# Kernel optimization log

Measured on AMD Instinct MI355X. Metric: run time of the kernel, lower is better.

The kernel has to match this reference:

```python
import jax, jax.numpy as jnp
import numpy as np

N_WIN = 7
DIM = 128
QK = 128
HEADS = 8
TOPK = 4


def _win(x, n_win):
    # (N, H, W, C) -> (N, n_win*n_win, h, w, C)
    N, H, W, C = x.shape
    h, w = H // n_win, W // n_win
    return x.reshape(N, n_win, h, n_win, w, C).transpose(0, 1, 3, 2, 4, 5).reshape(N, n_win * n_win, h, w, C)


def _unwin(x, n_win):
    # (N, p2, h, w, C) -> (N, H, W, C)
    N, p2, h, w, C = x.shape
    return x.reshape(N, n_win, n_win, h, w, C).transpose(0, 1, 3, 2, 4, 5).reshape(N, n_win * h, n_win * w, C)


def _dwconv(img_nhwc, k, b):
    # depthwise 3x3, SAME padding (LePE)
    x = img_nhwc.transpose(0, 3, 1, 2)
    y = jax.lax.conv_general_dilated(x, k, (1, 1), 'SAME',
                                     dimension_numbers=('NCHW', 'OIHW', 'NCHW'),
                                     feature_group_count=k.shape[0])
    y = y + b[None, :, None, None]
    return y.transpose(0, 2, 3, 1)


def _branch(xw, W, b):
    # xw: (N, p2, h, w, C); QKV linear + pixel/window-level views
    qkv = xw @ W + b
    q, kv = qkv[..., :QK], qkv[..., QK:]
    N, p2, h, w, _ = q.shape
    q_pix = q.reshape(N, p2, h * w, QK)
    kv_pix = kv.reshape(N, p2, h * w, QK + DIM)  # identity kv_down
    q_win = q.mean((2, 3))
    k_win = kv[..., :QK].mean((2, 3))
    return q_pix, kv_pix, q_win, k_win, kv


def _route(q_win, k_win, scale):
    # non-differentiable routing (detach) with Identity emb
    q = jax.lax.stop_gradient(q_win)
    k = jax.lax.stop_gradient(k_win)
    logit = (q * scale) @ k.transpose(0, 2, 1)  # (N, p2, p2)
    top_val, top_idx = jax.lax.top_k(logit, TOPK)
    r_weight = jax.nn.softmax(top_val, axis=-1)  # unused (mul_weight='none')
    return r_weight, top_idx


def _gather(kv_pix, idx):
    # kv_pix: (N, p2, w2, c), idx: (N, p2, K) -> (N, p2, K, w2, c)
    N = kv_pix.shape[0]
    bidx = jnp.arange(N)[:, None, None]
    return kv_pix[bidx, idx]


def _heads_q(q):
    # (N, p2, w2, m*c) -> (N, p2, m, w2, c)
    N, p2, w2, _ = q.shape
    return q.reshape(N, p2, w2, HEADS, -1).transpose(0, 1, 3, 2, 4)


def _heads_kv(kv):
    # (N, p2, K, w2, m*c) -> (N, p2, m, K*w2, c)
    N, p2, K, w2, _ = kv.shape
    return kv.reshape(N, p2, K, w2, HEADS, -1).transpose(0, 1, 4, 2, 3, 5).reshape(N, p2, HEADS, K * w2, -1)


def setup_inputs() -> dict:
    key = jax.random.key(0)
    ks = jax.random.split(key, 6)
    N, H, W = 8, 56, 56
    return {
        'x': jax.random.normal(ks[0], (N, H, W, DIM), jnp.float32),
        'y': jax.random.normal(ks[1], (N, H, W, DIM), jnp.float32),
        'w_qkv_x': jax.random.normal(ks[2], (DIM, 2 * QK + DIM), jnp.float32) * 0.02,
        'b_qkv_x': jnp.zeros((2 * QK + DIM,), jnp.float32),
        'w_qkv_y': jax.random.normal(ks[3], (DIM, 2 * QK + DIM), jnp.float32) * 0.02,
        'b_qkv_y': jnp.zeros((2 * QK + DIM,), jnp.float32),
        'w_lepe_x': jax.random.normal(ks[4], (DIM, 1, 3, 3), jnp.float32) * 0.1,
        'b_lepe_x': jnp.zeros((DIM,), jnp.float32),
        'w_lepe_y': jax.random.normal(ks[5], (DIM, 1, 3, 3), jnp.float32) * 0.1,
        'b_lepe_y': jnp.zeros((DIM,), jnp.float32),
    }


def reference(x, y, w_qkv_x, b_qkv_x, w_qkv_y, b_qkv_y, w_lepe_x, b_lepe_x, w_lepe_y, b_lepe_y):
    scale = QK ** (-0.5)
    N, H, W, C = x.shape
    h, w = H // N_WIN, W // N_WIN
    xw = _win(x, N_WIN)
    yw = _win(y, N_WIN)

    qx_pix, kvx_pix, qx_win, kx_win, kvx = _branch(xw, w_qkv_x, b_qkv_x)
    qy_pix, kvy_pix, qy_win, ky_win, kvy = _branch(yw, w_qkv_y, b_qkv_y)

    lepe_x = _dwconv(_unwin(kvx[..., QK:], N_WIN), w_lepe_x, b_lepe_x)
    lepe_y = _dwconv(_unwin(kvy[..., QK:], N_WIN), w_lepe_y, b_lepe_y)

    _, rx_idx = _route(qx_win, kx_win, scale)
    _, ry_idx = _route(qy_win, ky_win, scale)

    kvx_sel = _gather(kvx_pix, rx_idx)  # (N, p2, K, w2, QK+DIM)
    kvy_sel = _gather(kvy_pix, ry_idx)

    kx_sel, vx_sel = _heads_kv(kvx_sel[..., :QK]), _heads_kv(kvx_sel[..., QK:])
    ky_sel, vy_sel = _heads_kv(kvy_sel[..., :QK]), _heads_kv(kvy_sel[..., QK:])
    qx = _heads_q(qx_pix)
    qy = _heads_q(qy_pix)

    attn_x = jax.nn.softmax(jnp.einsum('bpmqc,bpmkc->bpmqk', qx * scale, kx_sel), axis=-1)
    attn_y = jax.nn.softmax(jnp.einsum('bpmqc,bpmkc->bpmqk', qy * scale, ky_sel), axis=-1)

    # cross attention: x-output uses y's attention weights on x's values, and vice versa
    out_x = jnp.einsum('bpmqk,bpmkc->bpmqc', attn_y, vx_sel)
    out_y = jnp.einsum('bpmqk,bpmkc->bpmqc', attn_x, vy_sel)

    p2 = N_WIN * N_WIN
    out_x = out_x.transpose(0, 1, 3, 2, 4).reshape(N, p2, h, w, DIM)
    out_y = out_y.transpose(0, 1, 3, 2, 4).reshape(N, p2, h, w, DIM)
    out_x = _unwin(out_x, N_WIN) + lepe_x
    out_y = _unwin(out_y, N_WIN) + lepe_y
    return (out_x, out_y)
```

## Files before the change

kernel.cpp:

```cpp
#include <hip/hip_runtime.h>

#define HWD 56
#define NWIN 7
#define P2 49
#define CIN 128
#define COUT 384
#define NB 8
#define SCALE 0.08838834764831843f

typedef __attribute__((ext_vector_type(8))) short bf16x8;
typedef __attribute__((ext_vector_type(4))) float f32x4;
typedef __attribute__((ext_vector_type(8))) unsigned short u16x8;
typedef unsigned short ushort_t;

__device__ inline unsigned short f2bf(float f) {
  unsigned int u = __float_as_uint(f);
  unsigned int r = (u + 0x7fffu + ((u >> 16) & 1u)) >> 16;
  return (unsigned short)r;
}
__device__ inline float bf2f(unsigned short b) {
  return __uint_as_float(((unsigned int)b) << 16);
}

__global__ __launch_bounds__(256) void meanproj_kernel(
    const float* __restrict__ xin, const float* __restrict__ yin,
    const float* __restrict__ Wx, const float* __restrict__ Bx,
    const float* __restrict__ Wy, const float* __restrict__ By,
    ushort_t* __restrict__ xbfx, ushort_t* __restrict__ xbfy,
    float* __restrict__ qwx, float* __restrict__ kwx,
    float* __restrict__ qwy, float* __restrict__ kwy)
{
  const int p = blockIdx.x, n = blockIdx.y, br = blockIdx.z;
  const float* X  = br ? yin : xin;
  const float* W  = br ? Wy  : Wx;
  const float* Bv = br ? By  : Bx;
  ushort_t* xb = (br ? xbfy : xbfx) + (size_t)(n * P2 + p) * 64 * CIN;
  float* qw = br ? qwy : qwx;
  float* kw = br ? kwy : kwx;

  __shared__ float sm[2][128];
  __shared__ float mxs[128];
  const int t = threadIdx.x;
  const int wr = p / NWIN, wc = p % NWIN;
  const int ch = t & 127, half = t >> 7;

  float s = 0.f;
#pragma unroll 4
  for (int i = 0; i < 32; ++i) {
    int pix = half * 32 + i;
    int a = wr * 8 + (pix >> 3), b = wc * 8 + (pix & 7);
    float v = X[(((size_t)n * HWD + a) * HWD + b) * CIN + ch];
    s += v;
    xb[pix * CIN + ch] = f2bf(v);
  }
  sm[half][ch] = s;
  __syncthreads();
  if (t < 128) mxs[t] = (sm[0][t] + sm[1][t]) * (1.f / 64.f);
  __syncthreads();

  float acc = Bv[t];
#pragma unroll 8
  for (int k = 0; k < 128; ++k) acc = fmaf(mxs[k], W[(size_t)k * COUT + t], acc);
  if (t < 128) qw[(n * P2 + p) * 128 + t] = acc;
  else         kw[(n * P2 + p) * 128 + (t - 128)] = acc;
}

__global__ __launch_bounds__(128) void wt_kernel(
    const float* __restrict__ Wx, const float* __restrict__ Wy,
    ushort_t* __restrict__ Wtx, ushort_t* __restrict__ Wty)
{
  const int br = blockIdx.y;
  const float* W = br ? Wy : Wx;
  ushort_t* Wt = br ? Wty : Wtx;
  const int c = blockIdx.x * 128 + threadIdx.x;
  for (int k8 = 0; k8 < 128; k8 += 8) {
    u16x8 buf;
#pragma unroll
    for (int i = 0; i < 8; ++i) buf[i] = f2bf(W[(size_t)(k8 + i) * COUT + c]);
    *(u16x8*)&Wt[(size_t)c * 128 + k8] = buf;
  }
}

__global__ __launch_bounds__(256) void route_kernel(
    const float* __restrict__ qwx, const float* __restrict__ kwx,
    const float* __restrict__ qwy, const float* __restrict__ kwy,
    int* __restrict__ idxx, int* __restrict__ idxy)
{
  const int br = blockIdx.x, n = blockIdx.y;
  const float* qw = br ? qwy : qwx;
  const float* kw = br ? kwy : kwx;
  int* idx = br ? idxy : idxx;

  __shared__ float qs[P2][128];
  __shared__ float ks[P2][128];
  __shared__ float ls[P2][52];
  const int t = threadIdx.x;
  for (int e = t; e < P2 * 128; e += 256) {
    qs[e >> 7][e & 127] = qw[(size_t)n * P2 * 128 + e];
    ks[e >> 7][e & 127] = kw[(size_t)n * P2 * 128 + e];
  }
  __syncthreads();
  for (int pair = t; pair < P2 * P2; pair += 256) {
    int r = pair / P2, j = pair % P2;
    float d = 0.f;
#pragma unroll
    for (int c4 = 0; c4 < 32; ++c4) {
      float4 a = *(const float4*)&qs[r][c4 * 4];
      float4 b = *(const float4*)&ks[j][c4 * 4];
      d = fmaf(a.x, b.x, d); d = fmaf(a.y, b.y, d);
      d = fmaf(a.z, b.z, d); d = fmaf(a.w, b.w, d);
    }
    ls[r][j] = d;
  }
  __syncthreads();
  if (t < P2) {
    int ch[4];
    for (int s = 0; s < 4; ++s) {
      float best = -1e30f; int bi = 0;
      for (int j = 0; j < P2; ++j) {
        bool taken = false;
        for (int u = 0; u < s; ++u) taken = taken || (ch[u] == j);
        if (!taken && ls[t][j] > best) { best = ls[t][j]; bi = j; }
      }
      ch[s] = bi;
      idx[((size_t)n * P2 + t) * 4 + s] = bi;
    }
  }
}

#define AS 136
__global__ __launch_bounds__(256) void qkv_gemm_kernel(
    const ushort_t* __restrict__ xbfx, const ushort_t* __restrict__ xbfy,
    const ushort_t* __restrict__ Wtx, const ushort_t* __restrict__ Wty,
    const float* __restrict__ Bx, const float* __restrict__ By,
    ushort_t* __restrict__ Qpx, ushort_t* __restrict__ Qpy,
    ushort_t* __restrict__ Kpx, ushort_t* __restrict__ Kpy,
    ushort_t* __restrict__ Vcx, ushort_t* __restrict__ Vcy,
    ushort_t* __restrict__ Vpx, ushort_t* __restrict__ Vpy)
{
  const int mt = blockIdx.x, nt = blockIdx.y, br = blockIdx.z;
  const ushort_t* Xb = br ? xbfy : xbfx;
  const ushort_t* Wt = br ? Wty : Wtx;
  const float* Bv = br ? By : Bx;

  __shared__ ushort_t a_s[128 * AS];
  __shared__ ushort_t b_s[128 * AS];

  const int t = threadIdx.x;
#pragma unroll
  for (int it = 0; it < 8; ++it) {
    int row = it * 16 + (t >> 4);
    int e8 = (t & 15) * 8;
    *(u16x8*)&a_s[row * AS + e8] = *(const u16x8*)&Xb[((size_t)mt * 128 + row) * 128 + e8];
    *(u16x8*)&b_s[row * AS + e8] = *(const u16x8*)&Wt[((size_t)nt * 128 + row) * 128 + e8];
  }
  __syncthreads();

  const int wv = t >> 6, wm = wv >> 1, wn = wv & 1;
  const int lane = t & 63, qd = lane >> 4, m16 = lane & 15;

  f32x4 acc[4][4];
#pragma unroll
  for (int i = 0; i < 4; ++i)
#pragma unroll
    for (int j = 0; j < 4; ++j) acc[i][j] = (f32x4){0.f, 0.f, 0.f, 0.f};

#pragma unroll
  for (int ks = 0; ks < 4; ++ks) {
    bf16x8 af[4], bfr[4];
#pragma unroll
    for (int fi = 0; fi < 4; ++fi)
      af[fi] = *(const bf16x8*)&a_s[(wm * 64 + fi * 16 + m16) * AS + ks * 32 + qd * 8];
#pragma unroll
    for (int fj = 0; fj < 4; ++fj)
      bfr[fj] = *(const bf16x8*)&b_s[(wn * 64 + fj * 16 + m16) * AS + ks * 32 + qd * 8];
#pragma unroll
    for (int fi = 0; fi < 4; ++fi)
#pragma unroll
      for (int fj = 0; fj < 4; ++fj)
        acc[fi][fj] = __builtin_amdgcn_mfma_f32_16x16x32_bf16(bfr[fj], af[fi], acc[fi][fj], 0, 0, 0);
  }

  const int gw = mt * 2 + wm;
  const float scl = (nt == 0) ? SCALE : 1.0f;

  if (nt < 2) {
    ushort_t* dst = (nt == 0) ? (br ? Qpy : Qpx) : (br ? Kpy : Kpx);
#pragma unroll
    for (int fj = 0; fj < 4; ++fj) {
      int lch = wn * 64 + fj * 16 + qd * 4;
      int h = lch >> 4, chlo = lch & 15;
      float4 b4 = *(const float4*)&Bv[nt * 128 + lch];
#pragma unroll
      for (int fi = 0; fi < 4; ++fi) {
        int pix = fi * 16 + m16;
        ushort4 st = {f2bf((acc[fi][fj][0] + b4.x) * scl), f2bf((acc[fi][fj][1] + b4.y) * scl),
                      f2bf((acc[fi][fj][2] + b4.z) * scl), f2bf((acc[fi][fj][3] + b4.w) * scl)};
        *(ushort4*)&dst[(((size_t)gw * 8 + h) * 64 + pix) * 16 + chlo] = st;
      }
    }
  } else {
    ushort_t* dvp = br ? Vpy : Vpx;
    ushort_t* dvc = br ? Vcy : Vcx;
#pragma unroll
    for (int fj = 0; fj < 4; ++fj) {
      int lch = wn * 64 + fj * 16 + qd * 4;
      int h = lch >> 4, chlo = lch & 15;
      float4 b4 = *(const float4*)&Bv[256 + lch];
#pragma unroll
      for (int fi = 0; fi < 4; ++fi) {
        int pix = fi * 16 + m16;
        float v0 = acc[fi][fj][0] + b4.x, v1 = acc[fi][fj][1] + b4.y;
        float v2 = acc[fi][fj][2] + b4.z, v3 = acc[fi][fj][3] + b4.w;
        ushort4 st = {f2bf(v0), f2bf(v1), f2bf(v2), f2bf(v3)};
        *(ushort4*)&dvp[(((size_t)gw * 8 + h) * 64 + pix) * 16 + chlo] = st;
        size_t cb = (((size_t)gw * 8 + h) * 16 + chlo) * 64 + pix;
        dvc[cb]        = st.x;
        dvc[cb + 64]   = st.y;
        dvc[cb + 128]  = st.z;
        dvc[cb + 192]  = st.w;
      }
    }
  }
}

__global__ __launch_bounds__(256) void attn_kernel(
    const ushort_t* __restrict__ Qpx, const ushort_t* __restrict__ Qpy,
    const ushort_t* __restrict__ Kpx, const ushort_t* __restrict__ Kpy,
    const ushort_t* __restrict__ Vcx, const ushort_t* __restrict__ Vcy,
    const ushort_t* __restrict__ Vpx, const ushort_t* __restrict__ Vpy,
    const int* __restrict__ idxx, const int* __restrict__ idxy,
    const float* __restrict__ wlx, const float* __restrict__ blx,
    const float* __restrict__ wly, const float* __restrict__ bly,
    float* __restrict__ dout)
{
  const int p = blockIdx.x, n = blockIdx.y, z = blockIdx.z;
  const int h = z >> 1, dir = z & 1;
  const ushort_t* Qp = dir ? Qpy : Qpx;
  const ushort_t* Kp = dir ? Kpy : Kpx;
  const ushort_t* Vc = dir ? Vcx : Vcy;
  const ushort_t* Vp = dir ? Vpx : Vpy;
  const int* idxK = dir ? idxy : idxx;
  const int* idxV = dir ? idxx : idxy;
  const float* wl = dir ? wlx : wly;
  const float* bl = dir ? blx : bly;
  const size_t OUTHALF = (size_t)NB * HWD * HWD * CIN;
  float* outp = dout + (dir ? 0 : OUTHALF);

  __shared__ float halo[100 * 20];
  __shared__ float wls[160];

  const int t = threadIdx.x;
  const int wv = t >> 6, r = t & 63;
  const int wr = p / NWIN, wc = p % NWIN;

  const int4 kidx = *(const int4*)&idxK[((size_t)n * P2 + p) * 4];
  const int4 vidx = *(const int4*)&idxV[((size_t)n * P2 + p) * 4];
  const int kw4[4] = {kidx.x, kidx.y, kidx.z, kidx.w};
  const int vw4[4] = {vidx.x, vidx.y, vidx.z, vidx.w};

  if (t < 200) {
    int hp = t >> 1, hf = t & 1;
    int A = wr * 8 - 1 + (int)((unsigned)hp / 10u);
    int B = wc * 8 - 1 + (int)((unsigned)hp % 10u);
    f32x4 f0 = {0.f, 0.f, 0.f, 0.f}, f1 = {0.f, 0.f, 0.f, 0.f};
    if ((unsigned)A < (unsigned)HWD && (unsigned)B < (unsigned)HWD) {
      int gw = (A >> 3) * NWIN + (B >> 3);
      int pix = (A & 7) * 8 + (B & 7);
      u16x8 vv = *(const u16x8*)&Vp[(((size_t)(n * P2 + gw) * 8 + h) * 64 + pix) * 16 + hf * 8];
      f0[0] = bf2f(vv[0]); f0[1] = bf2f(vv[1]); f0[2] = bf2f(vv[2]); f0[3] = bf2f(vv[3]);
      f1[0] = bf2f(vv[4]); f1[1] = bf2f(vv[5]); f1[2] = bf2f(vv[6]); f1[3] = bf2f(vv[7]);
    }
    *(f32x4*)&halo[hp * 20 + hf * 8] = f0;
    *(f32x4*)&halo[hp * 20 + hf * 8 + 4] = f1;
  }
  if (t < 160) {
    int row = t >> 4, c = t & 15;
    wls[t] = (row < 9) ? wl[(h * 16 + c) * 9 + row] : bl[h * 16 + c];
  }

  const int qd = r >> 4, m16 = r & 15;
  const f32x4 zf = {0.f, 0.f, 0.f, 0.f};

  const ushort_t* Qw = Qp + ((size_t)(n * P2 + p) * 8 + h) * 1024;
  bf16x8 qf = (bf16x8)(short)0;
  if (qd < 2) qf = *(const bf16x8*)&Qw[(wv * 16 + m16) * 16 + qd * 8];

  f32x4 s[8][2];
#pragma unroll
  for (int c = 0; c < 8; ++c) {
    const ushort_t* Kw = Kp + ((size_t)(n * P2 + kw4[c >> 1]) * 8 + h) * 1024;
    int lk = (c & 1) * 32;
    bf16x8 kf0 = (bf16x8)(short)0, kf1 = (bf16x8)(short)0;
    if (qd < 2) {
      kf0 = *(const bf16x8*)&Kw[(lk + m16) * 16 + qd * 8];
      kf1 = *(const bf16x8*)&Kw[(lk + 16 + m16) * 16 + qd * 8];
    }
    s[c][0] = __builtin_amdgcn_mfma_f32_16x16x32_bf16(kf0, qf, zf, 0, 0, 0);
    s[c][1] = __builtin_amdgcn_mfma_f32_16x16x32_bf16(kf1, qf, zf, 0, 0, 0);
  }

  float m = -1e30f;
#pragma unroll
  for (int c = 0; c < 8; ++c)
#pragma unroll
    for (int hh = 0; hh < 2; ++hh)
#pragma unroll
      for (int rr = 0; rr < 4; ++rr) m = fmaxf(m, s[c][hh][rr]);
  m = fmaxf(m, __shfl_xor(m, 16));
  m = fmaxf(m, __shfl_xor(m, 32));
  float l = 0.f;
#pragma unroll
  for (int c = 0; c < 8; ++c)
#pragma unroll
    for (int hh = 0; hh < 2; ++hh)
#pragma unroll
      for (int rr = 0; rr < 4; ++rr) {
        float e = __expf(s[c][hh][rr] - m);
        s[c][hh][rr] = e;
        l += e;
      }
  l += __shfl_xor(l, 16);
  l += __shfl_xor(l, 32);
  const float inv = 1.f / l;

  f32x4 oacc = {0.f, 0.f, 0.f, 0.f};
#pragma unroll
  for (int c = 0; c < 8; ++c) {
    int pk[4];
#pragma unroll
    for (int rr = 0; rr < 4; ++rr)
      pk[rr] = (int)((unsigned int)f2bf(s[c][0][rr]) | ((unsigned int)f2bf(s[c][1][rr]) << 16));
    u16x8 pfu;
#pragma unroll
    for (int j = 0; j < 8; ++j) {
      int srcl = (((qd & 1) * 2 + (j >> 2)) << 4) + m16;
      int w = __shfl(pk[j & 3], srcl);
      pfu[j] = (qd < 2) ? (unsigned short)(w & 0xffff) : (unsigned short)((unsigned)w >> 16);
    }
    const ushort_t* Vw = Vc + ((size_t)(n * P2 + vw4[c >> 1]) * 8 + h) * 1024;
    bf16x8 vtf = *(const bf16x8*)&Vw[m16 * 64 + (c & 1) * 32 + qd * 8];
    oacc = __builtin_amdgcn_mfma_f32_16x16x32_bf16(vtf, *(bf16x8*)&pfu, oacc, 0, 0, 0);
  }

  __syncthreads();

  const int pix = wv * 16 + m16;
  const int pa = pix >> 3, pb = pix & 7;

  f32x4 lep = *(const f32x4*)&wls[144 + qd * 4];
#pragma unroll
  for (int di = 0; di < 3; ++di)
#pragma unroll
    for (int dj = 0; dj < 3; ++dj) {
      f32x4 hv = *(const f32x4*)&halo[((pa + di) * 10 + pb + dj) * 20 + qd * 4];
      f32x4 wt4 = *(const f32x4*)&wls[(di * 3 + dj) * 16 + qd * 4];
#pragma unroll
      for (int rr = 0; rr < 4; ++rr) lep[rr] = fmaf(hv[rr], wt4[rr], lep[rr]);
    }

  const int ga = wr * 8 + pa, gb = wc * 8 + pb;
  float4 o = {oacc[0] * inv + lep[0], oacc[1] * inv + lep[1],
              oacc[2] * inv + lep[2], oacc[3] * inv + lep[3]};
  *(float4*)&outp[(((size_t)n * HWD + ga) * HWD + gb) * CIN + h * 16 + qd * 4] = o;
}

extern "C" void kernel_launch(void* const* d_in, const int* in_sizes, int n_in,
                              void* d_out, int out_size, void* d_ws, size_t ws_size,
                              hipStream_t stream) {
  const float* x        = (const float*)d_in[0];
  const float* y        = (const float*)d_in[1];
  const float* w_qkv_x  = (const float*)d_in[2];
  const float* b_qkv_x  = (const float*)d_in[3];
  const float* w_qkv_y  = (const float*)d_in[4];
  const float* b_qkv_y  = (const float*)d_in[5];
  const float* w_lepe_x = (const float*)d_in[6];
  const float* b_lepe_x = (const float*)d_in[7];
  const float* w_lepe_y = (const float*)d_in[8];
  const float* b_lepe_y = (const float*)d_in[9];
  float* out = (float*)d_out;

  const size_t hb_sz  = (size_t)NB * P2 * 8 * 64 * 16;
  const size_t xbf_sz = (size_t)NB * P2 * 64 * CIN;
  const size_t wt_sz  = (size_t)COUT * CIN;
  const size_t win_sz = (size_t)NB * P2 * 128;

  ushort_t* base = (ushort_t*)d_ws;
  ushort_t* Qpx = base;            ushort_t* Qpy = Qpx + hb_sz;
  ushort_t* Kpx = Qpy + hb_sz;     ushort_t* Kpy = Kpx + hb_sz;
  ushort_t* Vcx = Kpy + hb_sz;     ushort_t* Vcy = Vcx + hb_sz;
  ushort_t* Vpx = Vcy + hb_sz;     ushort_t* Vpy = Vpx + hb_sz;
  ushort_t* xbfx = Vpy + hb_sz;    ushort_t* xbfy = xbfx + xbf_sz;
  ushort_t* Wtx  = xbfy + xbf_sz;  ushort_t* Wty  = Wtx + wt_sz;
  float* qwx = (float*)(Wty + wt_sz);
  float* kwx = qwx + win_sz;
  float* qwy = kwx + win_sz;
  float* kwy = qwy + win_sz;
  int* idxx = (int*)(kwy + win_sz);
  int* idxy = idxx + NB * P2 * 4;

  meanproj_kernel<<<dim3(P2, NB, 2), 256, 0, stream>>>(
      x, y, w_qkv_x, b_qkv_x, w_qkv_y, b_qkv_y, xbfx, xbfy, qwx, kwx, qwy, kwy);
  wt_kernel<<<dim3(3, 2), 128, 0, stream>>>(w_qkv_x, w_qkv_y, Wtx, Wty);
  route_kernel<<<dim3(2, NB), 256, 0, stream>>>(qwx, kwx, qwy, kwy, idxx, idxy);
  qkv_gemm_kernel<<<dim3(196, 3, 2), 256, 0, stream>>>(
      xbfx, xbfy, Wtx, Wty, b_qkv_x, b_qkv_y,
      Qpx, Qpy, Kpx, Kpy, Vcx, Vcy, Vpx, Vpy);
  attn_kernel<<<dim3(P2, NB, 16), 256, 0, stream>>>(
      Qpx, Qpy, Kpx, Kpy, Vcx, Vcy, Vpx, Vpy, idxx, idxy,
      w_lepe_x, b_lepe_x, w_lepe_y, b_lepe_y, out);
}
```

Measured before the change: 231.5 us.

## Fuse weight transpose into meanproj, retile QKV GEMM per window, wave-parallel top-k

The weight transpose moves into meanproj_kernel (done by the p==0 blocks), which removes one kernel launch, and the window mean is now read with float4 loads. The QKV GEMM is retiled to one block per window, where each wave computes 96 output channels and reads weight fragments directly from global memory instead of through shared memory. Route top-k becomes a wave-wide shuffle/ballot reduction, and attention uses the 16x16x16 bf16 MFMA so no MMA lanes are wasted on zero padding. Grid order is swapped to batch-major. Risk: the weight loads in the GEMM are uncached global reads, and the fused transpose runs inside the same kernel that the GEMM later depends on.

```diff
diff --git a/kernel.cpp b/kernel.cpp
--- a/kernel.cpp
+++ b/kernel.cpp
@@ -13,6 +13,11 @@
 typedef __attribute__((ext_vector_type(8))) unsigned short u16x8;
 typedef unsigned short ushort_t;
 
+#if __has_builtin(__builtin_amdgcn_mfma_f32_16x16x16bf16_1k)
+#define HAVE_MFMA16 1
+typedef __attribute__((ext_vector_type(4))) short bf16x4;
+#endif
+
 __device__ inline unsigned short f2bf(float f) {
   unsigned int u = __float_as_uint(f);
   unsigned int r = (u + 0x7fffu + ((u >> 16) & 1u)) >> 16;
@@ -27,35 +32,42 @@
     const float* __restrict__ Wx, const float* __restrict__ Bx,
     const float* __restrict__ Wy, const float* __restrict__ By,
     ushort_t* __restrict__ xbfx, ushort_t* __restrict__ xbfy,
+    ushort_t* __restrict__ Wtx, ushort_t* __restrict__ Wty,
     float* __restrict__ qwx, float* __restrict__ kwx,
     float* __restrict__ qwy, float* __restrict__ kwy)
 {
-  const int p = blockIdx.x, n = blockIdx.y, br = blockIdx.z;
+  const int n = blockIdx.x, p = blockIdx.y, br = blockIdx.z;
   const float* X  = br ? yin : xin;
   const float* W  = br ? Wy  : Wx;
   const float* Bv = br ? By  : Bx;
   ushort_t* xb = (br ? xbfy : xbfx) + (size_t)(n * P2 + p) * 64 * CIN;
+  ushort_t* Wt = br ? Wty : Wtx;
   float* qw = br ? qwy : qwx;
   float* kw = br ? kwy : kwx;
 
-  __shared__ float sm[2][128];
+  __shared__ float smf[8][132];
   __shared__ float mxs[128];
   const int t = threadIdx.x;
   const int wr = p / NWIN, wc = p % NWIN;
-  const int ch = t & 127, half = t >> 7;
-
-  float s = 0.f;
-#pragma unroll 4
-  for (int i = 0; i < 32; ++i) {
-    int pix = half * 32 + i;
-    int a = wr * 8 + (pix >> 3), b = wc * 8 + (pix & 7);
-    float v = X[(((size_t)n * HWD + a) * HWD + b) * CIN + ch];
-    s += v;
-    xb[pix * CIN + ch] = f2bf(v);
-  }
-  sm[half][ch] = s;
-  __syncthreads();
-  if (t < 128) mxs[t] = (sm[0][t] + sm[1][t]) * (1.f / 64.f);
+  const int ch4 = (t & 31) * 4, pg = t >> 5;
+
+  const float* Xrow = X + (((size_t)n * HWD + wr * 8 + pg) * HWD + wc * 8) * CIN;
+  float4 s4 = {0.f, 0.f, 0.f, 0.f};
+#pragma unroll
+  for (int i = 0; i < 8; ++i) {
+    float4 v = *(const float4*)&Xrow[i * CIN + ch4];
+    s4.x += v.x; s4.y += v.y; s4.z += v.z; s4.w += v.w;
+    ushort4 o = {f2bf(v.x), f2bf(v.y), f2bf(v.z), f2bf(v.w)};
+    *(ushort4*)&xb[(pg * 8 + i) * CIN + ch4] = o;
+  }
+  *(float4*)&smf[pg][ch4] = s4;
+  __syncthreads();
+  if (t < 128) {
+    float s = 0.f;
+#pragma unroll
+    for (int g = 0; g < 8; ++g) s += smf[g][t];
+    mxs[t] = s * (1.f / 64.f);
+  }
   __syncthreads();
 
   float acc = Bv[t];
@@ -63,21 +75,12 @@
   for (int k = 0; k < 128; ++k) acc = fmaf(mxs[k], W[(size_t)k * COUT + t], acc);
   if (t < 128) qw[(n * P2 + p) * 128 + t] = acc;
   else         kw[(n * P2 + p) * 128 + (t - 128)] = acc;
-}
-
-__global__ __launch_bounds__(128) void wt_kernel(
-    const float* __restrict__ Wx, const float* __restrict__ Wy,
-    ushort_t* __restrict__ Wtx, ushort_t* __restrict__ Wty)
-{
-  const int br = blockIdx.y;
-  const float* W = br ? Wy : Wx;
-  ushort_t* Wt = br ? Wty : Wtx;
-  const int c = blockIdx.x * 128 + threadIdx.x;
-  for (int k8 = 0; k8 < 128; k8 += 8) {
-    u16x8 buf;
-#pragma unroll
-    for (int i = 0; i < 8; ++i) buf[i] = f2bf(W[(size_t)(k8 + i) * COUT + c]);
-    *(u16x8*)&Wt[(size_t)c * 128 + k8] = buf;
+
+  if (p == 0) {
+    for (int e = t; e < 48 * 128; e += 256) {
+      int c = n * 48 + (e >> 7), k = e & 127;
+      Wt[(size_t)c * 128 + k] = f2bf(W[(size_t)k * COUT + c]);
+    }
   }
 }
 
@@ -113,22 +116,28 @@
     ls[r][j] = d;
   }
   __syncthreads();
-  if (t < P2) {
-    int ch[4];
-    for (int s = 0; s < 4; ++s) {
-      float best = -1e30f; int bi = 0;
-      for (int j = 0; j < P2; ++j) {
-        bool taken = false;
-        for (int u = 0; u < s; ++u) taken = taken || (ch[u] == j);
-        if (!taken && ls[t][j] > best) { best = ls[t][j]; bi = j; }
-      }
-      ch[s] = bi;
-      idx[((size_t)n * P2 + t) * 4 + s] = bi;
-    }
-  }
-}
-
-#define AS 136
+  const int lane = t & 63, wv = t >> 6;
+  for (int row = wv; row < P2; row += 4) {
+    float v = (lane < P2) ? ls[row][lane] : -1e30f;
+    int out4[4];
+#pragma unroll
+    for (int sel = 0; sel < 4; ++sel) {
+      float m = v;
+#pragma unroll
+      for (int msk = 1; msk < 64; msk <<= 1) m = fmaxf(m, __shfl_xor(m, msk));
+      unsigned long long b = __ballot(v == m);
+      int bi = __ffsll((unsigned long long)b) - 1;
+      out4[sel] = bi;
+      if (lane == bi) v = -1e30f;
+    }
+    if (lane == 0) {
+      int4 o = {out4[0], out4[1], out4[2], out4[3]};
+      *(int4*)&idx[((size_t)n * P2 + row) * 4] = o;
+    }
+  }
+}
+
+#define XS 136
 __global__ __launch_bounds__(256) void qkv_gemm_kernel(
     const ushort_t* __restrict__ xbfx, const ushort_t* __restrict__ xbfy,
     const ushort_t* __restrict__ Wtx, const ushort_t* __restrict__ Wty,
@@ -138,87 +147,73 @@
     ushort_t* __restrict__ Vcx, ushort_t* __restrict__ Vcy,
     ushort_t* __restrict__ Vpx, ushort_t* __restrict__ Vpy)
 {
-  const int mt = blockIdx.x, nt = blockIdx.y, br = blockIdx.z;
-  const ushort_t* Xb = br ? xbfy : xbfx;
+  const int n = blockIdx.x, p = blockIdx.y, br = blockIdx.z;
+  const ushort_t* Xw = (br ? xbfy : xbfx) + (size_t)(n * P2 + p) * 64 * CIN;
   const ushort_t* Wt = br ? Wty : Wtx;
   const float* Bv = br ? By : Bx;
-
-  __shared__ ushort_t a_s[128 * AS];
-  __shared__ ushort_t b_s[128 * AS];
+  ushort_t* Qp = br ? Qpy : Qpx;
+  ushort_t* Kp = br ? Kpy : Kpx;
+  ushort_t* Vc = br ? Vcy : Vcx;
+  ushort_t* Vp = br ? Vpy : Vpx;
+
+  __shared__ ushort_t a_s[64 * XS];
 
   const int t = threadIdx.x;
 #pragma unroll
-  for (int it = 0; it < 8; ++it) {
-    int row = it * 16 + (t >> 4);
-    int e8 = (t & 15) * 8;
-    *(u16x8*)&a_s[row * AS + e8] = *(const u16x8*)&Xb[((size_t)mt * 128 + row) * 128 + e8];
-    *(u16x8*)&b_s[row * AS + e8] = *(const u16x8*)&Wt[((size_t)nt * 128 + row) * 128 + e8];
-  }
-  __syncthreads();
-
-  const int wv = t >> 6, wm = wv >> 1, wn = wv & 1;
-  const int lane = t & 63, qd = lane >> 4, m16 = lane & 15;
-
-  f32x4 acc[4][4];
+  for (int it = 0; it < 4; ++it) {
+    int e = it * 256 + t;
+    int row = e >> 4, c8 = (e & 15) * 8;
+    *(u16x8*)&a_s[row * XS + c8] = *(const u16x8*)&Xw[row * 128 + c8];
+  }
+  __syncthreads();
+
+  const int wv = t >> 6, lane = t & 63, qd = lane >> 4, m16 = lane & 15;
+  const ushort_t* Wb = Wt + (size_t)(wv * 96) * 128;
+
+  f32x4 acc[4][6];
 #pragma unroll
   for (int i = 0; i < 4; ++i)
 #pragma unroll
-    for (int j = 0; j < 4; ++j) acc[i][j] = (f32x4){0.f, 0.f, 0.f, 0.f};
+    for (int j = 0; j < 6; ++j) acc[i][j] = (f32x4){0.f, 0.f, 0.f, 0.f};
 
 #pragma unroll
   for (int ks = 0; ks < 4; ++ks) {
-    bf16x8 af[4], bfr[4];
+    bf16x8 af[4], bfw[6];
 #pragma unroll
     for (int fi = 0; fi < 4; ++fi)
-      af[fi] = *(const bf16x8*)&a_s[(wm * 64 + fi * 16 + m16) * AS + ks * 32 + qd * 8];
-#pragma unroll
-    for (int fj = 0; fj < 4; ++fj)
-      bfr[fj] = *(const bf16x8*)&b_s[(wn * 64 + fj * 16 + m16) * AS + ks * 32 + qd * 8];
+      af[fi] = *(const bf16x8*)&a_s[(fi * 16 + m16) * XS + ks * 32 + qd * 8];
+#pragma unroll
+    for (int fj = 0; fj < 6; ++fj)
+      bfw[fj] = *(const bf16x8*)&Wb[(size_t)(fj * 16 + m16) * 128 + ks * 32 + qd * 8];
 #pragma unroll
     for (int fi = 0; fi < 4; ++fi)
 #pragma unroll
-      for (int fj = 0; fj < 4; ++fj)
-        acc[fi][fj] = __builtin_amdgcn_mfma_f32_16x16x32_bf16(bfr[fj], af[fi], acc[fi][fj], 0, 0, 0);
-  }
-
-  const int gw = mt * 2 + wm;
-  const float scl = (nt == 0) ? SCALE : 1.0f;
-
-  if (nt < 2) {
-    ushort_t* dst = (nt == 0) ? (br ? Qpy : Qpx) : (br ? Kpy : Kpx);
-#pragma unroll
-    for (int fj = 0; fj < 4; ++fj) {
-      int lch = wn * 64 + fj * 16 + qd * 4;
-      int h = lch >> 4, chlo = lch & 15;
-      float4 b4 = *(const float4*)&Bv[nt * 128 + lch];
-#pragma unroll
-      for (int fi = 0; fi < 4; ++fi) {
-        int pix = fi * 16 + m16;
-        ushort4 st = {f2bf((acc[fi][fj][0] + b4.x) * scl), f2bf((acc[fi][fj][1] + b4.y) * scl),
-                      f2bf((acc[fi][fj][2] + b4.z) * scl), f2bf((acc[fi][fj][3] + b4.w) * scl)};
-        *(ushort4*)&dst[(((size_t)gw * 8 + h) * 64 + pix) * 16 + chlo] = st;
-      }
-    }
-  } else {
-    ushort_t* dvp = br ? Vpy : Vpx;
-    ushort_t* dvc = br ? Vcy : Vcx;
-#pragma unroll
-    for (int fj = 0; fj < 4; ++fj) {
-      int lch = wn * 64 + fj * 16 + qd * 4;
-      int h = lch >> 4, chlo = lch & 15;
-      float4 b4 = *(const float4*)&Bv[256 + lch];
-#pragma unroll
-      for (int fi = 0; fi < 4; ++fi) {
-        int pix = fi * 16 + m16;
-        float v0 = acc[fi][fj][0] + b4.x, v1 = acc[fi][fj][1] + b4.y;
-        float v2 = acc[fi][fj][2] + b4.z, v3 = acc[fi][fj][3] + b4.w;
-        ushort4 st = {f2bf(v0), f2bf(v1), f2bf(v2), f2bf(v3)};
-        *(ushort4*)&dvp[(((size_t)gw * 8 + h) * 64 + pix) * 16 + chlo] = st;
-        size_t cb = (((size_t)gw * 8 + h) * 16 + chlo) * 64 + pix;
-        dvc[cb]        = st.x;
-        dvc[cb + 64]   = st.y;
-        dvc[cb + 128]  = st.z;
-        dvc[cb + 192]  = st.w;
+      for (int fj = 0; fj < 6; ++fj)
+        acc[fi][fj] = __builtin_amdgcn_mfma_f32_16x16x32_bf16(bfw[fj], af[fi], acc[fi][fj], 0, 0, 0);
+  }
+
+  const size_t wb = (size_t)(n * P2 + p) * 8;
+#pragma unroll
+  for (int fj = 0; fj < 6; ++fj) {
+    const int ch = wv * 96 + fj * 16 + qd * 4;
+    float4 b4 = *(const float4*)&Bv[ch];
+    const int isQ = ch < 128, isK = (ch >= 128) && (ch < 256);
+    const float scl = isQ ? SCALE : 1.0f;
+    const int lch = ch & 127, h = lch >> 4, chlo = lch & 15;
+#pragma unroll
+    for (int fi = 0; fi < 4; ++fi) {
+      int pix = fi * 16 + m16;
+      float v0 = (acc[fi][fj][0] + b4.x) * scl, v1 = (acc[fi][fj][1] + b4.y) * scl;
+      float v2 = (acc[fi][fj][2] + b4.z) * scl, v3 = (acc[fi][fj][3] + b4.w) * scl;
+      ushort4 st = {f2bf(v0), f2bf(v1), f2bf(v2), f2bf(v3)};
+      if (isQ) {
+        *(ushort4*)&Qp[((wb + h) * 64 + pix) * 16 + chlo] = st;
+      } else if (isK) {
+        *(ushort4*)&Kp[((wb + h) * 64 + pix) * 16 + chlo] = st;
+      } else {
+        *(ushort4*)&Vp[((wb + h) * 64 + pix) * 16 + chlo] = st;
+        size_t cb = ((wb + h) * 16 + chlo) * 64 + pix;
+        Vc[cb] = st.x; Vc[cb + 64] = st.y; Vc[cb + 128] = st.z; Vc[cb + 192] = st.w;
       }
     }
   }
@@ -234,7 +229,7 @@
     const float* __restrict__ wly, const float* __restrict__ bly,
     float* __restrict__ dout)
 {
-  const int p = blockIdx.x, n = blockIdx.y, z = blockIdx.z;
+  const int n = blockIdx.x, p = blockIdx.y, z = blockIdx.z;
   const int h = z >> 1, dir = z & 1;
   const ushort_t* Qp = dir ? Qpy : Qpx;
   const ushort_t* Kp = dir ? Kpy : Kpx;
@@ -251,7 +246,7 @@
   __shared__ float wls[160];
 
   const int t = threadIdx.x;
-  const int wv = t >> 6, r = t & 63;
+  const int wv = t >> 6;
   const int wr = p / NWIN, wc = p % NWIN;
 
   const int4 kidx = *(const int4*)&idxK[((size_t)n * P2 + p) * 4];
@@ -279,14 +274,25 @@
     wls[t] = (row < 9) ? wl[(h * 16 + c) * 9 + row] : bl[h * 16 + c];
   }
 
-  const int qd = r >> 4, m16 = r & 15;
+  const int lane = t & 63, qd = lane >> 4, m16 = lane & 15;
   const f32x4 zf = {0.f, 0.f, 0.f, 0.f};
-
   const ushort_t* Qw = Qp + ((size_t)(n * P2 + p) * 8 + h) * 1024;
+
+  f32x4 s[8][2];
+#if HAVE_MFMA16
+  bf16x4 qf = *(const bf16x4*)&Qw[(wv * 16 + m16) * 16 + qd * 4];
+#pragma unroll
+  for (int c = 0; c < 8; ++c) {
+    const ushort_t* Kw = Kp + ((size_t)(n * P2 + kw4[c >> 1]) * 8 + h) * 1024;
+    int lk = (c & 1) * 32;
+    bf16x4 kf0 = *(const bf16x4*)&Kw[(lk + m16) * 16 + qd * 4];
+    bf16x4 kf1 = *(const bf16x4*)&Kw[(lk + 16 + m16) * 16 + qd * 4];
+    s[c][0] = __builtin_amdgcn_mfma_f32_16x16x16bf16_1k(kf0, qf, zf, 0, 0, 0);
+    s[c][1] = __builtin_amdgcn_mfma_f32_16x16x16bf16_1k(kf1, qf, zf, 0, 0, 0);
+  }
+#else
   bf16x8 qf = (bf16x8)(short)0;
   if (qd < 2) qf = *(const bf16x8*)&Qw[(wv * 16 + m16) * 16 + qd * 8];
-
-  f32x4 s[8][2];
 #pragma unroll
   for (int c = 0; c < 8; ++c) {
     const ushort_t* Kw = Kp + ((size_t)(n * P2 + kw4[c >> 1]) * 8 + h) * 1024;
@@ -299,6 +305,7 @@
     s[c][0] = __builtin_amdgcn_mfma_f32_16x16x32_bf16(kf0, qf, zf, 0, 0, 0);
     s[c][1] = __builtin_amdgcn_mfma_f32_16x16x32_bf16(kf1, qf, zf, 0, 0, 0);
   }
+#endif
 
   float m = -1e30f;
 #pragma unroll
@@ -399,14 +406,14 @@
   int* idxx = (int*)(kwy + win_sz);
   int* idxy = idxx + NB * P2 * 4;
 
-  meanproj_kernel<<<dim3(P2, NB, 2), 256, 0, stream>>>(
-      x, y, w_qkv_x, b_qkv_x, w_qkv_y, b_qkv_y, xbfx, xbfy, qwx, kwx, qwy, kwy);
-  wt_kernel<<<dim3(3, 2), 128, 0, stream>>>(w_qkv_x, w_qkv_y, Wtx, Wty);
+  meanproj_kernel<<<dim3(NB, P2, 2), 256, 0, stream>>>(
+      x, y, w_qkv_x, b_qkv_x, w_qkv_y, b_qkv_y, xbfx, xbfy, Wtx, Wty,
+      qwx, kwx, qwy, kwy);
   route_kernel<<<dim3(2, NB), 256, 0, stream>>>(qwx, kwx, qwy, kwy, idxx, idxy);
-  qkv_gemm_kernel<<<dim3(196, 3, 2), 256, 0, stream>>>(
+  qkv_gemm_kernel<<<dim3(NB, P2, 2), 256, 0, stream>>>(
       xbfx, xbfy, Wtx, Wty, b_qkv_x, b_qkv_y,
       Qpx, Qpy, Kpx, Kpy, Vcx, Vcy, Vpx, Vpy);
-  attn_kernel<<<dim3(P2, NB, 16), 256, 0, stream>>>(
+  attn_kernel<<<dim3(NB, P2, 16), 256, 0, stream>>>(
       Qpx, Qpy, Kpx, Kpy, Vcx, Vcy, Vpx, Vpy, idxx, idxy,
       w_lepe_x, b_lepe_x, w_lepe_y, b_lepe_y, out);
 }
```

After: 221.0 us. -4.6%, faster.
